# Kernel optimization log

Measured on AMD Instinct MI355X. Metric: run time of the kernel, lower is better.

The kernel has to match this reference:

```python
import jax, jax.numpy as jnp
import numpy as np

N_FEATURES = 26          # number of feature categories (FEATURE_AND_ENCODER entries)
VOCAB_PER_FEATURE = 50000  # ids in [f*V, (f+1)*V) belong to feature f
SLOTS_PER_FEATURE = 8
BATCH = 16384
EMBED = 32
VOCAB = N_FEATURES * VOCAB_PER_FEATURE


def setup_inputs() -> dict:
    key = jax.random.key(0)
    ks = jax.random.split(key, 8)
    P = N_FEATURES * SLOTS_PER_FEATURE  # 208 ids per row
    x = jax.random.randint(ks[0], (BATCH, P), 0, VOCAB, dtype=jnp.int64)
    table = jax.random.normal(ks[1], (VOCAB, EMBED), dtype=jnp.float32) * 0.1
    D = N_FEATURES * EMBED  # 832
    W0 = jax.random.normal(ks[2], (D, 64), dtype=jnp.float32) * (1.0 / np.sqrt(D))
    b0 = jax.random.normal(ks[3], (64,), dtype=jnp.float32) * 0.01
    W1 = jax.random.normal(ks[4], (64, 16), dtype=jnp.float32) * (1.0 / 8.0)
    b1 = jax.random.normal(ks[5], (16,), dtype=jnp.float32) * 0.01
    W2 = jax.random.normal(ks[6], (16, 1), dtype=jnp.float32) * 0.25
    return {"x": x, "table": table, "W0": W0, "b0": b0, "W1": W1, "b1": b1, "W2": W2}


def reference(x, table, W0, b0, W1, b1, W2):
    B = x.shape[0]
    # dynamic embedding lookup: [B, P, E]
    embeds = table[x]
    # category of each id (what encoder.match_category encodes): [B, P]
    cat = x // VOCAB_PER_FEATURE
    # mask+gather+reduce_sum per feature == one-hot segment sum over features
    onehot = jax.nn.one_hot(cat, N_FEATURES, dtype=table.dtype)  # [B, P, F]
    pooled = jnp.einsum('bpe,bpf->bfe', embeds, onehot)          # [B, F, E]
    feats = pooled.reshape(B, N_FEATURES * EMBED)                # concat of per-feature sums
    h = jax.nn.relu(feats @ W0 + b0)
    h = jax.nn.relu(h @ W1 + b1)
    logits = h @ W2
    return jax.nn.sigmoid(logits)
```

## Files before the change

kernel.cpp:

```cpp
#include <hip/hip_runtime.h>
#include <math.h>

#define BATCH 16384
#define PP    208
#define NF    26
#define VPF   50000u
#define EMB   32
#define DD    832

typedef __attribute__((ext_vector_type(8))) short short8v;
typedef __attribute__((ext_vector_type(4))) float float4v;

static __device__ __forceinline__ ushort f32_to_bf16(float f) {
    unsigned u = __builtin_bit_cast(unsigned, f);
    unsigned r = (u + 0x7fffu + ((u >> 16) & 1u)) >> 16;
    return (ushort)r;
}

__global__ __launch_bounds__(256) void prep_kernel(const float* __restrict__ W0,
                                                   ushort* __restrict__ w0p) {
    const int i = blockIdx.x * 256 + threadIdx.x;
    if (i < DD * 64) {
        const int k = i >> 6, c = i & 63;
        const int kt = k >> 5, kk = k & 31;
        w0p[(kt * 64 + c) * 32 + kk] = f32_to_bf16(W0[i]);
    }
}

__global__ __launch_bounds__(256, 8) void pool_kernel(const int* __restrict__ x,
                                                      const float* __restrict__ table,
                                                      ushort* __restrict__ feats) {
    __shared__ int   s_ids[PP];
    __shared__ float s_pool[DD];

    const int    tid = threadIdx.x;
    const size_t row = blockIdx.x;

    for (int i = tid; i < DD; i += 256) s_pool[i] = 0.0f;
    if (tid < PP) s_ids[tid] = x[row * PP + tid];
    __syncthreads();

    const int e  = tid & 31;
    const int p0 = (tid >> 5) * 26;
    float* pool  = s_pool + e;

#pragma unroll 1
    for (int b = 0; b < 24; b += 4) {
        const unsigned id0 = (unsigned)s_ids[p0 + b + 0];
        const unsigned id1 = (unsigned)s_ids[p0 + b + 1];
        const unsigned id2 = (unsigned)s_ids[p0 + b + 2];
        const unsigned id3 = (unsigned)s_ids[p0 + b + 3];
        const float v0 = table[(size_t)id0 * EMB + e];
        const float v1 = table[(size_t)id1 * EMB + e];
        const float v2 = table[(size_t)id2 * EMB + e];
        const float v3 = table[(size_t)id3 * EMB + e];
        atomicAdd(pool + (id0 / VPF) * EMB, v0);
        atomicAdd(pool + (id1 / VPF) * EMB, v1);
        atomicAdd(pool + (id2 / VPF) * EMB, v2);
        atomicAdd(pool + (id3 / VPF) * EMB, v3);
    }
    {
        const unsigned idA = (unsigned)s_ids[p0 + 24];
        const unsigned idB = (unsigned)s_ids[p0 + 25];
        const float vA = table[(size_t)idA * EMB + e];
        const float vB = table[(size_t)idB * EMB + e];
        atomicAdd(pool + (idA / VPF) * EMB, vA);
        atomicAdd(pool + (idB / VPF) * EMB, vB);
    }
    __syncthreads();

    if (tid < DD / 4) {
        ushort4 o;
        o.x = f32_to_bf16(s_pool[tid * 4 + 0]);
        o.y = f32_to_bf16(s_pool[tid * 4 + 1]);
        o.z = f32_to_bf16(s_pool[tid * 4 + 2]);
        o.w = f32_to_bf16(s_pool[tid * 4 + 3]);
        *reinterpret_cast<ushort4*>(feats + row * DD + tid * 4) = o;
    }
}

__global__ __launch_bounds__(256) void mlp_kernel(const ushort* __restrict__ feats,
                                                  const ushort* __restrict__ w0p,
                                                  const float* __restrict__ b0,
                                                  const float* __restrict__ W1,
                                                  const float* __restrict__ b1,
                                                  const float* __restrict__ W2,
                                                  float* __restrict__ out) {
    __shared__ float sH[64][65];
    __shared__ float sH1[64][17];

    const int tid   = threadIdx.x;
    const int wave  = tid >> 6;
    const int lane  = tid & 63;
    const int lrow  = lane & 15;
    const int lk    = lane >> 4;
    const int brow0 = blockIdx.x * 64;

    float4v acc[4];
#pragma unroll
    for (int n = 0; n < 4; ++n) acc[n] = (float4v){0.f, 0.f, 0.f, 0.f};

    const ushort* frow  = feats + (size_t)(brow0 + wave * 16 + lrow) * DD + lk * 8;
    const ushort* wbase = w0p + lrow * 32 + lk * 8;

#pragma unroll 2
    for (int kt = 0; kt < 26; ++kt) {
        const short8v a = *reinterpret_cast<const short8v*>(frow + kt * 32);
#pragma unroll
        for (int n = 0; n < 4; ++n) {
            const short8v b = *reinterpret_cast<const short8v*>(wbase + (size_t)(kt * 64 + n * 16) * 32);
            acc[n] = __builtin_amdgcn_mfma_f32_16x16x32_bf16(a, b, acc[n], 0, 0, 0);
        }
    }

#pragma unroll
    for (int n = 0; n < 4; ++n) {
        const int   col = n * 16 + lrow;
        const float bb  = b0[col];
#pragma unroll
        for (int r = 0; r < 4; ++r) {
            const int rr = wave * 16 + lk * 4 + r;
            sH[rr][col] = fmaxf(acc[n][r] + bb, 0.f);
        }
    }
    __syncthreads();

    {
        const int r = tid >> 2, cg = (tid & 3) * 4;
        float a0 = b1[cg + 0], a1 = b1[cg + 1], a2 = b1[cg + 2], a3 = b1[cg + 3];
#pragma unroll 8
        for (int k = 0; k < 64; ++k) {
            const float  h  = sH[r][k];
            const float4 wv = *reinterpret_cast<const float4*>(W1 + k * 16 + cg);
            a0 = fmaf(h, wv.x, a0);
            a1 = fmaf(h, wv.y, a1);
            a2 = fmaf(h, wv.z, a2);
            a3 = fmaf(h, wv.w, a3);
        }
        sH1[r][cg + 0] = fmaxf(a0, 0.f);
        sH1[r][cg + 1] = fmaxf(a1, 0.f);
        sH1[r][cg + 2] = fmaxf(a2, 0.f);
        sH1[r][cg + 3] = fmaxf(a3, 0.f);
    }
    __syncthreads();

    if (tid < 64) {
        float z = 0.f;
#pragma unroll
        for (int j = 0; j < 16; ++j) z = fmaf(sH1[tid][j], W2[j], z);
        out[brow0 + tid] = 1.f / (1.f + expf(-z));
    }
}

extern "C" void kernel_launch(void* const* d_in, const int* in_sizes, int n_in,
                              void* d_out, int out_size, void* d_ws, size_t ws_size,
                              hipStream_t stream) {
    const int*   x     = (const int*)d_in[0];
    const float* table = (const float*)d_in[1];
    const float* W0    = (const float*)d_in[2];
    const float* b0    = (const float*)d_in[3];
    const float* W1    = (const float*)d_in[4];
    const float* b1    = (const float*)d_in[5];
    const float* W2    = (const float*)d_in[6];
    float*       out   = (float*)d_out;

    ushort* feats16 = (ushort*)d_ws;
    ushort* w0p     = feats16 + (size_t)BATCH * DD;

    prep_kernel<<<(DD * 64 + 255) / 256, 256, 0, stream>>>(W0, w0p);
    pool_kernel<<<BATCH, 256, 0, stream>>>(x, table, feats16);
    mlp_kernel<<<BATCH / 64, 256, 0, stream>>>(feats16, w0p, b0, W1, b1, W2, out);
}
```

Measured before the change: 756.1 us.

## Convert embedding table to bf16 and restructure pooling and MLP kernels

Adds a per-call pass that converts the whole embedding table to bf16 in workspace. The pooling kernel then gathers 4-byte bf16 pairs per lane, with 16 lanes per id and all 13 loads issued before the atomics, and loads ids with vector loads. The MLP kernel now handles 16 rows per block with a split-K across two waves, register double-buffering of operands, and bias/ReLU folded into the second layer. The table conversion reads and writes the full table every call (about 166MB read, 83MB written), which may cost more than the gather bandwidth it saves, and it also lowers embedding precision.

```diff
diff --git a/kernel.cpp b/kernel.cpp
--- a/kernel.cpp
+++ b/kernel.cpp
@@ -7,6 +7,7 @@
 #define VPF   50000u
 #define EMB   32
 #define DD    832
+#define VOCAB (NF * 50000)
 
 typedef __attribute__((ext_vector_type(8))) short short8v;
 typedef __attribute__((ext_vector_type(4))) float float4v;
@@ -16,9 +17,26 @@
     unsigned r = (u + 0x7fffu + ((u >> 16) & 1u)) >> 16;
     return (ushort)r;
 }
-
-__global__ __launch_bounds__(256) void prep_kernel(const float* __restrict__ W0,
-                                                   ushort* __restrict__ w0p) {
+static __device__ __forceinline__ unsigned pack_bf16x2(float lo, float hi) {
+    return (unsigned)f32_to_bf16(lo) | ((unsigned)f32_to_bf16(hi) << 16);
+}
+
+__global__ __launch_bounds__(256) void prep_tbl(const float* __restrict__ table,
+                                                ushort* __restrict__ tbl16) {
+    const size_t i = ((size_t)blockIdx.x * 256 + threadIdx.x) * 8;
+    if (i >= (size_t)VOCAB * EMB) return;
+    const float4 a = *reinterpret_cast<const float4*>(table + i);
+    const float4 b = *reinterpret_cast<const float4*>(table + i + 4);
+    uint4 o;
+    o.x = pack_bf16x2(a.x, a.y);
+    o.y = pack_bf16x2(a.z, a.w);
+    o.z = pack_bf16x2(b.x, b.y);
+    o.w = pack_bf16x2(b.z, b.w);
+    *reinterpret_cast<uint4*>(tbl16 + i) = o;
+}
+
+__global__ __launch_bounds__(256) void prep_w0(const float* __restrict__ W0,
+                                               ushort* __restrict__ w0p) {
     const int i = blockIdx.x * 256 + threadIdx.x;
     if (i < DD * 64) {
         const int k = i >> 6, c = i & 63;
@@ -27,8 +45,8 @@
     }
 }
 
-__global__ __launch_bounds__(256, 8) void pool_kernel(const int* __restrict__ x,
-                                                      const float* __restrict__ table,
+__global__ __launch_bounds__(256, 4) void pool_kernel(const int* __restrict__ x,
+                                                      const ushort* __restrict__ tbl,
                                                       ushort* __restrict__ feats) {
     __shared__ int   s_ids[PP];
     __shared__ float s_pool[DD];
@@ -37,7 +55,57 @@
     const size_t row = blockIdx.x;
 
     for (int i = tid; i < DD; i += 256) s_pool[i] = 0.0f;
-    if (tid < PP) s_ids[tid] = x[row * PP + tid];
+    if (tid < PP / 4)
+        reinterpret_cast<int4*>(s_ids)[tid] =
+            reinterpret_cast<const int4*>(x + row * PP)[tid];
+    __syncthreads();
+
+    const int g = tid >> 4;
+    const int l = tid & 15;
+
+    unsigned ids[13];
+#pragma unroll
+    for (int p = 0; p < 13; ++p) ids[p] = (unsigned)s_ids[p * 16 + g];
+
+    unsigned vals[13];
+#pragma unroll
+    for (int p = 0; p < 13; ++p)
+        vals[p] = *reinterpret_cast<const unsigned*>(tbl + (size_t)ids[p] * EMB + 2 * l);
+
+    float* pool = s_pool + 2 * l;
+#pragma unroll
+    for (int p = 0; p < 13; ++p) {
+        const unsigned cat = ids[p] / VPF;
+        const float f0 = __builtin_bit_cast(float, vals[p] << 16);
+        const float f1 = __builtin_bit_cast(float, vals[p] & 0xffff0000u);
+        atomicAdd(pool + cat * EMB + 0, f0);
+        atomicAdd(pool + cat * EMB + 1, f1);
+    }
+    __syncthreads();
+
+    if (tid < DD / 4) {
+        ushort4 o;
+        o.x = f32_to_bf16(s_pool[tid * 4 + 0]);
+        o.y = f32_to_bf16(s_pool[tid * 4 + 1]);
+        o.z = f32_to_bf16(s_pool[tid * 4 + 2]);
+        o.w = f32_to_bf16(s_pool[tid * 4 + 3]);
+        *reinterpret_cast<ushort4*>(feats + row * DD + tid * 4) = o;
+    }
+}
+
+__global__ __launch_bounds__(256, 4) void pool_kernel_f32(const int* __restrict__ x,
+                                                          const float* __restrict__ table,
+                                                          ushort* __restrict__ feats) {
+    __shared__ int   s_ids[PP];
+    __shared__ float s_pool[DD];
+
+    const int    tid = threadIdx.x;
+    const size_t row = blockIdx.x;
+
+    for (int i = tid; i < DD; i += 256) s_pool[i] = 0.0f;
+    if (tid < PP / 4)
+        reinterpret_cast<int4*>(s_ids)[tid] =
+            reinterpret_cast<const int4*>(x + row * PP)[tid];
     __syncthreads();
 
     const int e  = tid & 31;
@@ -79,72 +147,91 @@
     }
 }
 
-__global__ __launch_bounds__(256) void mlp_kernel(const ushort* __restrict__ feats,
+__global__ __launch_bounds__(128) void mlp_kernel(const ushort* __restrict__ feats,
                                                   const ushort* __restrict__ w0p,
                                                   const float* __restrict__ b0,
                                                   const float* __restrict__ W1,
                                                   const float* __restrict__ b1,
                                                   const float* __restrict__ W2,
                                                   float* __restrict__ out) {
-    __shared__ float sH[64][65];
-    __shared__ float sH1[64][17];
+    __shared__ float sC[16][68];
+    __shared__ float sH1[16][17];
+    __shared__ float sB0[64];
 
     const int tid   = threadIdx.x;
-    const int wave  = tid >> 6;
+    const int wid   = tid >> 6;
     const int lane  = tid & 63;
     const int lrow  = lane & 15;
     const int lk    = lane >> 4;
-    const int brow0 = blockIdx.x * 64;
+    const int brow0 = blockIdx.x * 16;
+
+    if (tid < 64) sB0[tid] = b0[tid];
 
     float4v acc[4];
 #pragma unroll
     for (int n = 0; n < 4; ++n) acc[n] = (float4v){0.f, 0.f, 0.f, 0.f};
 
-    const ushort* frow  = feats + (size_t)(brow0 + wave * 16 + lrow) * DD + lk * 8;
+    const int kt0 = wid * 13;
+    const ushort* frow  = feats + (size_t)(brow0 + lrow) * DD + lk * 8;
     const ushort* wbase = w0p + lrow * 32 + lk * 8;
 
-#pragma unroll 2
-    for (int kt = 0; kt < 26; ++kt) {
-        const short8v a = *reinterpret_cast<const short8v*>(frow + kt * 32);
-#pragma unroll
-        for (int n = 0; n < 4; ++n) {
-            const short8v b = *reinterpret_cast<const short8v*>(wbase + (size_t)(kt * 64 + n * 16) * 32);
-            acc[n] = __builtin_amdgcn_mfma_f32_16x16x32_bf16(a, b, acc[n], 0, 0, 0);
+    short8v a_cur, a_nxt;
+    short8v b_cur[4], b_nxt[4];
+    a_cur = *reinterpret_cast<const short8v*>(frow + kt0 * 32);
+#pragma unroll
+    for (int n = 0; n < 4; ++n)
+        b_cur[n] = *reinterpret_cast<const short8v*>(wbase + (size_t)(kt0 * 64 + n * 16) * 32);
+
+#pragma unroll
+    for (int i = 0; i < 13; ++i) {
+        if (i < 12) {
+            const int kt = kt0 + i + 1;
+            a_nxt = *reinterpret_cast<const short8v*>(frow + kt * 32);
+#pragma unroll
+            for (int n = 0; n < 4; ++n)
+                b_nxt[n] = *reinterpret_cast<const short8v*>(wbase + (size_t)(kt * 64 + n * 16) * 32);
         }
-    }
-
-#pragma unroll
-    for (int n = 0; n < 4; ++n) {
-        const int   col = n * 16 + lrow;
-        const float bb  = b0[col];
-#pragma unroll
-        for (int r = 0; r < 4; ++r) {
-            const int rr = wave * 16 + lk * 4 + r;
-            sH[rr][col] = fmaxf(acc[n][r] + bb, 0.f);
-        }
+#pragma unroll
+        for (int n = 0; n < 4; ++n)
+            acc[n] = __builtin_amdgcn_mfma_f32_16x16x32_bf16(a_cur, b_cur[n], acc[n], 0, 0, 0);
+        a_cur = a_nxt;
+#pragma unroll
+        for (int n = 0; n < 4; ++n) b_cur[n] = b_nxt[n];
+    }
+
+    if (wid == 0) {
+#pragma unroll
+        for (int n = 0; n < 4; ++n)
+#pragma unroll
+            for (int r = 0; r < 4; ++r)
+                sC[lk * 4 + r][n * 16 + lrow] = acc[n][r];
+    }
+    __syncthreads();
+    if (wid == 1) {
+#pragma unroll
+        for (int n = 0; n < 4; ++n)
+#pragma unroll
+            for (int r = 0; r < 4; ++r)
+                sC[lk * 4 + r][n * 16 + lrow] += acc[n][r];
     }
     __syncthreads();
 
     {
-        const int r = tid >> 2, cg = (tid & 3) * 4;
-        float a0 = b1[cg + 0], a1 = b1[cg + 1], a2 = b1[cg + 2], a3 = b1[cg + 3];
+        const int r = tid >> 3, c = (tid & 7) * 2;
+        float a0 = b1[c], a1 = b1[c + 1];
 #pragma unroll 8
         for (int k = 0; k < 64; ++k) {
-            const float  h  = sH[r][k];
-            const float4 wv = *reinterpret_cast<const float4*>(W1 + k * 16 + cg);
+            const float h = fmaxf(sC[r][k] + sB0[k], 0.f);
+            const float2 wv = *reinterpret_cast<const float2*>(W1 + k * 16 + c);
             a0 = fmaf(h, wv.x, a0);
             a1 = fmaf(h, wv.y, a1);
-            a2 = fmaf(h, wv.z, a2);
-            a3 = fmaf(h, wv.w, a3);
         }
-        sH1[r][cg + 0] = fmaxf(a0, 0.f);
-        sH1[r][cg + 1] = fmaxf(a1, 0.f);
-        sH1[r][cg + 2] = fmaxf(a2, 0.f);
-        sH1[r][cg + 3] = fmaxf(a3, 0.f);
-    }
-    __syncthreads();
-
-    if (tid < 64) {
+        sH1[r][c + 0] = fmaxf(a0, 0.f);
+        sH1[r][c + 1] = fmaxf(a1, 0.f);
+    }
+    __syncthreads();
+
+    if (tid < 16) {
         float z = 0.f;
 #pragma unroll
         for (int j = 0; j < 16; ++j) z = fmaf(sH1[tid][j], W2[j], z);
@@ -166,8 +253,18 @@
 
     ushort* feats16 = (ushort*)d_ws;
     ushort* w0p     = feats16 + (size_t)BATCH * DD;
-
-    prep_kernel<<<(DD * 64 + 255) / 256, 256, 0, stream>>>(W0, w0p);
-    pool_kernel<<<BATCH, 256, 0, stream>>>(x, table, feats16);
-    mlp_kernel<<<BATCH / 64, 256, 0, stream>>>(feats16, w0p, b0, W1, b1, W2, out);
-}
+    ushort* tbl16   = w0p + (size_t)DD * 64;
+    const size_t need = ((size_t)BATCH * DD + (size_t)DD * 64 + (size_t)VOCAB * EMB) * 2;
+
+    prep_w0<<<(DD * 64 + 255) / 256, 256, 0, stream>>>(W0, w0p);
+
+    if (ws_size >= need) {
+        const int nconv = ((int)((size_t)VOCAB * EMB / 8) + 255) / 256;
+        prep_tbl<<<nconv, 256, 0, stream>>>(table, tbl16);
+        pool_kernel<<<BATCH, 256, 0, stream>>>(x, tbl16, feats16);
+    } else {
+        pool_kernel_f32<<<BATCH, 256, 0, stream>>>(x, table, feats16);
+    }
+
+    mlp_kernel<<<BATCH / 16, 128, 0, stream>>>(feats16, w0p, b0, W1, b1, W2, out);
+}
```

Result: slower. 815.5 us (+7.9%).
